# Kernel tuning notes

Measured on AMD Instinct MI355X. Metric: run time of the kernel, lower is better.

## Reference

```python
import jax, jax.numpy as jnp
import numpy as np

K = 256       # num states
M = 2         # markov order
D = 256       # lemb_size
V = 50000     # ntypes (vocab)
T = 512
B = 256
Kp1 = K + 1
EPS = 1e-5
INIT = 0.1


def _layernorm(h, g, b):
    mu = h.mean(-1, keepdims=True)
    var = ((h - mu) ** 2).mean(-1, keepdims=True)
    return (h - mu) / jnp.sqrt(var + EPS) * g + b


def setup_inputs() -> dict:
    key = jax.random.key(0)
    ks = jax.random.split(key, 12)
    u = lambda k, shp: jax.random.uniform(k, shp, jnp.float32, -INIT, INIT)
    return {
        "x": jax.random.randint(ks[0], (T, B), 0, V, dtype=jnp.int32),
        "z": jax.random.randint(ks[1], (T, B), 0, K, dtype=jnp.int32),
        "lembs": u(ks[2], (K, D)),
        "tlembs": u(ks[3], (Kp1, D)),
        "dec_W": u(ks[4], (V, D)),
        "dec_b": jnp.zeros((V,), jnp.float32),
        "em_W": u(ks[5], (D, D)),
        "em_bias": jnp.zeros((D,), jnp.float32),
        "em_g": jnp.ones((D,), jnp.float32),
        "em_beta": jnp.zeros((D,), jnp.float32),
        "td_W": u(ks[6], (K, M * D)),
        "td_b": jnp.zeros((K,), jnp.float32),
        "tm_W": u(ks[7], (M * D, M * D)),
        "tm_bias": jnp.zeros((M * D,), jnp.float32),
        "tn_g": jnp.ones((M * D,), jnp.float32),
        "tn_beta": jnp.zeros((M * D,), jnp.float32),
    }


def reference(x, z, lembs, tlembs, dec_W, dec_b, em_W, em_bias, em_g, em_beta,
              td_W, td_b, tm_W, tm_bias, tn_g, tn_beta):
    # --- emission distribution: K x V log-normalized ---
    h = _layernorm(lembs + jax.nn.relu(lembs @ em_W.T + em_bias), em_g, em_beta)
    emdist = jax.nn.log_softmax(h @ dec_W.T + dec_b, axis=1)  # (K, V)

    # --- transition distribution: (Kp1^M, K) log-normalized ---
    # cartesian product of label embeddings, row-major: row r <-> (i_0,...,i_{M-1})
    idx = jnp.indices((Kp1,) * M).reshape(M, -1)                 # (M, Kp1^M)
    cat = tlembs[idx].transpose(1, 0, 2).reshape(-1, M * D)      # (Kp1^M, M*D)
    th = _layernorm(cat + jax.nn.relu(cat @ tm_W.T + tm_bias), tn_g, tn_beta)
    transdist = jax.nn.log_softmax(th @ td_W.T + td_b, axis=1)   # (Kp1^M, K)

    # --- log_joint ---
    xlps = emdist.T[x]                                           # (T, B, K)
    emlps = jnp.take_along_axis(xlps, z[..., None].astype(jnp.int32), axis=2)[..., 0].sum(0)  # (B,)

    zpad = jnp.concatenate([jnp.full((M, B), K, dtype=z.dtype), z], axis=0)  # (T+M, B)
    win = jnp.stack([zpad[m:m + T] for m in range(M + 1)], 0)    # (M+1, T, B)
    lin = win[0]
    for m in range(1, M):
        lin = lin * Kp1 + win[m]                                 # row index into (Kp1^M, K)
    trans_lps = transdist[lin, win[M]]                           # (T, B)
    return emlps + trans_lps.sum(0)                              # (B,)
```

## Files before the change

### kernel.cpp

```cpp
#include <hip/hip_runtime.h>

#define Kst 256
#define Dd 256
#define Vv 50000
#define VPAD 50176
#define Tt 512
#define Bb 256
#define KP1 257
#define MD 512
#define NROWS (KP1*KP1)
#define EPSf 1e-5f

#define VB2 196
#define NP1 (VB2*4)
#define NTR ((NROWS+31)/32)
#define EMB 800

typedef __attribute__((ext_vector_type(8))) short short8;
typedef __attribute__((ext_vector_type(4))) float f32x4;
typedef __attribute__((ext_vector_type(4))) unsigned u32x4;
typedef __attribute__((ext_vector_type(2))) unsigned u32x2;

__device__ __forceinline__ unsigned short f2bf(float f) {
    unsigned u = __builtin_bit_cast(unsigned, f);
    unsigned r = (u + 0x7fffu + ((u >> 16) & 1u)) >> 16;
    return (unsigned short)r;
}
__device__ __forceinline__ float bf2f(unsigned short u) {
    return __builtin_bit_cast(float, ((unsigned)u) << 16);
}
__device__ __forceinline__ unsigned bfpack(float lo, float hi) {
    return __builtin_amdgcn_perm(__builtin_bit_cast(unsigned, hi),
                                 __builtin_bit_cast(unsigned, lo), 0x07060302u);
}
__device__ __forceinline__ unsigned f2bf2(float lo, float hi) {
    return (unsigned)f2bf(lo) | ((unsigned)f2bf(hi) << 16);
}

union HPU {
    struct { short ta[32][264]; float lsep[4][32][2]; float musig[32][2]; } g;
    struct { short pl[64][266]; } p;
};

__global__ __launch_bounds__(256) void k_hP(
    const float* __restrict__ lembs, const float* __restrict__ em_W,
    const float* __restrict__ em_bias, const float* __restrict__ em_g,
    const float* __restrict__ em_beta, unsigned short* __restrict__ h_bf,
    const float* __restrict__ tlembs, const float* __restrict__ tm_W,
    float* __restrict__ P0, float* __restrict__ P1,
    const float* __restrict__ td_W, const float* __restrict__ tn_g,
    const float* __restrict__ tn_beta, const float* __restrict__ td_b,
    unsigned short* __restrict__ tdwg_bf, float* __restrict__ Gt,
    float* __restrict__ Bt, const float* __restrict__ dec_W,
    unsigned short* __restrict__ dwP)
{
    __shared__ HPU su;
    int bid = blockIdx.x;
    int tid = threadIdx.x, lane = tid & 63, wv = tid >> 6;
    int l15 = lane & 15, q = lane >> 4;

    if (bid >= 108) {
        int pb = bid - 108;
        int vb2 = pb >> 2, c = pb & 3;
        short (*pl)[266] = su.p.pl;
        int base_row = vb2*256 + c*64;
        #pragma unroll 4
        for (int i = 0; i < 16; ++i) {
            int row = wv*16 + i;
            int grow = base_row + row; if (grow > Vv-1) grow = Vv-1;
            float4 f = ((const float4*)(dec_W + (size_t)grow*Dd))[lane];
            u32x2 w; w.x = bfpack(f.x, f.y); w.y = bfpack(f.z, f.w);
            *(u32x2*)&pl[row][lane*4] = w;
        }
        __syncthreads();
        #pragma unroll
        for (int i = 0; i < 8; ++i) {
            short8 val = *(const short8*)&pl[(lane & 15)*4 + wv][i*32 + (lane >> 4)*8];
            *(short8*)(dwP + ((size_t)vb2*8192 + (size_t)i*1024
                              + (c*4 + wv)*64 + lane)*8) = val;
        }
        return;
    }

    if (bid >= 44) {
        int c = (bid - 44)*4 + wv;
        const float4* w4 = (const float4*)(td_W + (size_t)c*MD);
        const float4* g4 = (const float4*)tn_g;
        const float4* b4 = (const float4*)tn_beta;
        float sg = 0.f, sb = 0.f;
        short8 o;
        #pragma unroll
        for (int u = 0; u < 2; ++u) {
            int j4 = lane*2 + u;
            float4 w = w4[j4], g = g4[j4], bt = b4[j4];
            sg += w.x*g.x + w.y*g.y + w.z*g.z + w.w*g.w;
            sb += w.x*bt.x + w.y*bt.y + w.z*bt.z + w.w*bt.w;
            o[u*4+0] = (short)f2bf(w.x*g.x);
            o[u*4+1] = (short)f2bf(w.y*g.y);
            o[u*4+2] = (short)f2bf(w.z*g.z);
            o[u*4+3] = (short)f2bf(w.w*g.w);
        }
        {
            int wvv = c >> 6, l15v = (c >> 2) & 15, ctv = c & 3;
            int ksv = lane >> 2, qv = lane & 3;
            *(short8*)(tdwg_bf +
                ((((size_t)wvv*16 + ksv)*4 + ctv)*64 + (qv*16 + l15v))*8) = o;
        }
        #pragma unroll
        for (int dd = 32; dd > 0; dd >>= 1) {
            sg += __shfl_xor(sg, dd);
            sb += __shfl_xor(sb, dd);
        }
        if (lane == 0) { Gt[c] = sg; Bt[c] = sb + td_b[c]; }
        return;
    }

    short (*ta)[264] = su.g.ta;
    float (*lsep)[32][2] = su.g.lsep;
    float (*musig)[2] = su.g.musig;

    int job, r0, cb, koff, BK;
    const float* Arow; const float* Brow;
    if (bid < 8) {
        job = 0; r0 = bid*32; cb = 0; koff = 0; BK = Dd;
        Arow = lembs; Brow = em_W;
    } else {
        int b2 = bid - 8;
        int half = b2 / 18;
        int b3 = b2 % 18;
        job = 1 + half;
        r0 = (b3 >> 1) * 32;
        cb = (b3 & 1) * 256;
        koff = half * 256; BK = MD;
        Arow = tlembs; Brow = tm_W;
    }

    {
        int row = tid >> 3, seg = (tid & 7) * 32;
        int r = r0 + row;
        if (r > 256) r = 256;
        const float4* s4 = (const float4*)(Arow + (size_t)r*Dd + seg);
        #pragma unroll
        for (int u = 0; u < 4; ++u) {
            float4 f0 = s4[u*2], f1 = s4[u*2+1];
            u32x4 pk;
            pk.x = bfpack(f0.x, f0.y);
            pk.y = bfpack(f0.z, f0.w);
            pk.z = bfpack(f1.x, f1.y);
            pk.w = bfpack(f1.z, f1.w);
            *(short8*)&ta[row][seg + u*8] = __builtin_bit_cast(short8, pk);
        }
    }
    __syncthreads();

    const float* bptr[4];
    #pragma unroll
    for (int ct = 0; ct < 4; ++ct) {
        int j = cb + wv*64 + ct*16 + l15;
        bptr[ct] = Brow + (size_t)j*BK + koff + q*8;
    }
    f32x4 acc[2][4];
    #pragma unroll
    for (int rt = 0; rt < 2; ++rt)
        #pragma unroll
        for (int ct = 0; ct < 4; ++ct)
            acc[rt][ct] = (f32x4){0.f,0.f,0.f,0.f};
    for (int ks = 0; ks < 8; ++ks) {
        short8 a0 = *(const short8*)&ta[ 0 + l15][ks*32 + q*8];
        short8 a1 = *(const short8*)&ta[16 + l15][ks*32 + q*8];
        short8 b[4];
        #pragma unroll
        for (int ct = 0; ct < 4; ++ct) {
            float4 f0 = *(const float4*)(bptr[ct] + ks*32);
            float4 f1 = *(const float4*)(bptr[ct] + ks*32 + 4);
            u32x4 pk;
            pk.x = bfpack(f0.x, f0.y);
            pk.y = bfpack(f0.z, f0.w);
            pk.z = bfpack(f1.x, f1.y);
            pk.w = bfpack(f1.z, f1.w);
            b[ct] = __builtin_bit_cast(short8, pk);
        }
        #pragma unroll
        for (int ct = 0; ct < 4; ++ct) {
            acc[0][ct] = __builtin_amdgcn_mfma_f32_16x16x32_bf16(a0, b[ct], acc[0][ct], 0,0,0);
            acc[1][ct] = __builtin_amdgcn_mfma_f32_16x16x32_bf16(a1, b[ct], acc[1][ct], 0,0,0);
        }
    }

    if (job != 0) {
        float* Pd = (job == 1) ? P0 : P1;
        #pragma unroll
        for (int rt = 0; rt < 2; ++rt) {
            #pragma unroll
            for (int reg = 0; reg < 4; ++reg) {
                int r = r0 + rt*16 + q*4 + reg;
                if (r < KP1) {
                    float* dst = Pd + (size_t)r*MD + cb + wv*64;
                    #pragma unroll
                    for (int ct = 0; ct < 4; ++ct)
                        dst[ct*16 + l15] = acc[rt][ct][reg];
                }
            }
        }
        return;
    }

    float bias_c[4];
    #pragma unroll
    for (int ct = 0; ct < 4; ++ct)
        bias_c[ct] = em_bias[wv*64 + ct*16 + l15];
    #pragma unroll
    for (int rt = 0; rt < 2; ++rt) {
        #pragma unroll
        for (int reg = 0; reg < 4; ++reg) {
            int r = r0 + rt*16 + q*4 + reg;
            #pragma unroll
            for (int ct = 0; ct < 4; ++ct) {
                float lv = lembs[(size_t)r*Dd + wv*64 + ct*16 + l15];
                acc[rt][ct][reg] = lv + fmaxf(acc[rt][ct][reg] + bias_c[ct], 0.f);
            }
        }
    }
    #pragma unroll
    for (int rt = 0; rt < 2; ++rt) {
        #pragma unroll
        for (int reg = 0; reg < 4; ++reg) {
            float s  = ((acc[rt][0][reg] + acc[rt][1][reg]) + (acc[rt][2][reg] + acc[rt][3][reg]));
            float ss = ((acc[rt][0][reg]*acc[rt][0][reg] + acc[rt][1][reg]*acc[rt][1][reg])
                      + (acc[rt][2][reg]*acc[rt][2][reg] + acc[rt][3][reg]*acc[rt][3][reg]));
            s  += __shfl_xor(s, 1);  ss += __shfl_xor(ss, 1);
            s  += __shfl_xor(s, 2);  ss += __shfl_xor(ss, 2);
            s  += __shfl_xor(s, 4);  ss += __shfl_xor(ss, 4);
            s  += __shfl_xor(s, 8);  ss += __shfl_xor(ss, 8);
            if (l15 == 0) {
                int rw = rt*16 + q*4 + reg;
                lsep[wv][rw][0] = s;
                lsep[wv][rw][1] = ss;
            }
        }
    }
    __syncthreads();
    if (tid < 32) {
        float s  = (lsep[0][tid][0] + lsep[1][tid][0]) + (lsep[2][tid][0] + lsep[3][tid][0]);
        float ss = (lsep[0][tid][1] + lsep[1][tid][1]) + (lsep[2][tid][1] + lsep[3][tid][1]);
        float mu = s * (1.f/Dd);
        musig[tid][0] = mu;
        musig[tid][1] = rsqrtf(ss*(1.f/Dd) - mu*mu + EPSf);
    }
    __syncthreads();
    float gl[4], bl[4];
    #pragma unroll
    for (int ct = 0; ct < 4; ++ct) {
        gl[ct] = em_g[wv*64 + ct*16 + l15];
        bl[ct] = em_beta[wv*64 + ct*16 + l15];
    }
    #pragma unroll
    for (int rt = 0; rt < 2; ++rt) {
        #pragma unroll
        for (int reg = 0; reg < 4; ++reg) {
            int rw = rt*16 + q*4 + reg;
            int r = r0 + rw;
            float mu = musig[rw][0], rs = musig[rw][1];
            unsigned short* dst = h_bf + (size_t)r*Dd + wv*64;
            #pragma unroll
            for (int ct = 0; ct < 4; ++ct)
                dst[ct*16 + l15] = f2bf((acc[rt][ct][reg] - mu)*rs*gl[ct] + bl[ct]);
        }
    }
}

union SMemU {
    struct { short hs[64][264]; } em;
    struct { short th[32][520]; float musig[32][2]; float lsep[4][32][2]; } tr;
};

__global__ __launch_bounds__(256, 4) void k_emtrans(
    const unsigned short* __restrict__ dwP, const float* __restrict__ dec_b,
    const unsigned short* __restrict__ h_bf, float* __restrict__ part1,
    unsigned short* __restrict__ E2,
    const float* __restrict__ tlembs, const float* __restrict__ P0,
    const float* __restrict__ P1, const float* __restrict__ tm_bias,
    const short* __restrict__ tdwg_bf, const float* __restrict__ Gt,
    const float* __restrict__ Bt, float* __restrict__ lse_t,
    unsigned short* __restrict__ Td)
{
    __shared__ SMemU sm;
    int bid = blockIdx.x;
    int tid = threadIdx.x, lane = tid & 63, wv = tid >> 6;
    int l15 = lane & 15, q = lane >> 4;

    if (bid < EMB) {
        int xcd = bid & 7, slot = bid >> 3;
        int g2 = slot >> 2, kg = slot & 3;
        int vb = g2*8 + xcd;
        if (vb >= VB2) return;
        short (*hs)[264] = sm.em.hs;

        {
            int row = tid >> 2, c0 = (tid & 3) * 64;
            const short8* src = (const short8*)(h_bf + (size_t)(kg*64 + row)*Dd + c0);
            #pragma unroll
            for (int u = 0; u < 8; ++u)
                *(short8*)&hs[row][c0 + u*8] = src[u];
        }
        __syncthreads();

        f32x4 acc[4][4];
        #pragma unroll
        for (int mt = 0; mt < 4; ++mt)
            #pragma unroll
            for (int ct = 0; ct < 4; ++ct)
                acc[mt][ct] = (f32x4){0.f,0.f,0.f,0.f};

        const short8* bb8 = (const short8*)dwP + ((size_t)vb*8*16 + wv*4)*64 + lane;
        short8 Bf[3][4];
        #define LDB_EM(slot_, kk) { \
            Bf[slot_][0] = bb8[((kk)*16 + 0)*64]; \
            Bf[slot_][1] = bb8[((kk)*16 + 1)*64]; \
            Bf[slot_][2] = bb8[((kk)*16 + 2)*64]; \
            Bf[slot_][3] = bb8[((kk)*16 + 3)*64]; }
        LDB_EM(0, 0)
        LDB_EM(1, 1)
        #pragma unroll
        for (int ks = 0; ks < 8; ++ks) {
            if (ks < 6) LDB_EM((ks+2)%3, ks+2)
            short8 a[4];
            #pragma unroll
            for (int mt = 0; mt < 4; ++mt)
                a[mt] = *(const short8*)&hs[mt*16 + l15][ks*32 + q*8];
            #pragma unroll
            for (int mt = 0; mt < 4; ++mt)
                #pragma unroll
                for (int ct = 0; ct < 4; ++ct)
                    acc[mt][ct] = __builtin_amdgcn_mfma_f32_16x16x32_bf16(a[mt], Bf[ks%3][ct], acc[mt][ct], 0,0,0);
        }
        #undef LDB_EM

        int vcol[4]; bool vok[4];
        #pragma unroll
        for (int ct = 0; ct < 4; ++ct) {
            int v = vb*256 + wv*64 + l15*4 + ct;
            vok[ct] = (v < Vv);
            vcol[ct] = v < Vv ? v : Vv-1;
        }
        #pragma unroll
        for (int ct = 0; ct < 4; ++ct) {
            if (vok[ct]) {
                float db = dec_b[vcol[ct]];
                #pragma unroll
                for (int mt = 0; mt < 4; ++mt)
                    #pragma unroll
                    for (int reg = 0; reg < 4; ++reg)
                        acc[mt][ct][reg] += db;
            } else {
                #pragma unroll
                for (int mt = 0; mt < 4; ++mt)
                    #pragma unroll
                    for (int reg = 0; reg < 4; ++reg)
                        acc[mt][ct][reg] = -1e30f;
            }
        }
        #pragma unroll
        for (int mt = 0; mt < 4; ++mt) {
            #pragma unroll
            for (int reg = 0; reg < 4; ++reg) {
                int k = kg*64 + mt*16 + q*4 + reg;
                u32x2 p;
                p.x = f2bf2(acc[mt][0][reg], acc[mt][1][reg]);
                p.y = f2bf2(acc[mt][2][reg], acc[mt][3][reg]);
                *(u32x2*)(E2 + (size_t)k*VPAD + vb*256 + wv*64 + l15*4) = p;
            }
        }
        #pragma unroll
        for (int mt = 0; mt < 4; ++mt) {
            #pragma unroll
            for (int reg = 0; reg < 4; ++reg) {
                float s = (__expf(acc[mt][0][reg]) + __expf(acc[mt][1][reg]))
                        + (__expf(acc[mt][2][reg]) + __expf(acc[mt][3][reg]));
                s += __shfl_xor(s, 1);
                s += __shfl_xor(s, 2);
                s += __shfl_xor(s, 4);
                s += __shfl_xor(s, 8);
                if (l15 == 0) {
                    int k = kg*64 + mt*16 + q*4 + reg;
                    part1[(size_t)(vb*4 + wv)*256 + k] = s;
                }
            }
        }
        return;
    }

    int tr_id = bid - EMB;
    if (tr_id >= NTR) return;
    short (*th)[520]   = sm.tr.th;
    float (*musig)[2]  = sm.tr.musig;
    float (*lsep)[32][2] = sm.tr.lsep;
    int r0 = tr_id * 32;

    {
        const float4* bias0 = (const float4*)tm_bias;
        const float4* bias1 = (const float4*)(tm_bias + 256);
        float4 c0 = bias0[lane], c1 = bias1[lane];
        int i0a[8], i1a[8];
        #pragma unroll
        for (int i = 0; i < 8; ++i) {
            int r = r0 + wv*8 + i; if (r >= NROWS) r = NROWS - 1;
            i0a[i] = r / KP1; i1a[i] = r - i0a[i]*KP1;
        }
        #define ROWBODY(i, A0, B0, T0, A1, B1, T1) { \
            int row = wv*8 + (i); \
            float v0 = (T0).x + fmaxf((A0).x+(B0).x+c0.x, 0.f); \
            float v1 = (T0).y + fmaxf((A0).y+(B0).y+c0.y, 0.f); \
            float v2 = (T0).z + fmaxf((A0).z+(B0).z+c0.z, 0.f); \
            float v3 = (T0).w + fmaxf((A0).w+(B0).w+c0.w, 0.f); \
            float v4 = (T1).x + fmaxf((A1).x+(B1).x+c1.x, 0.f); \
            float v5 = (T1).y + fmaxf((A1).y+(B1).y+c1.y, 0.f); \
            float v6 = (T1).z + fmaxf((A1).z+(B1).z+c1.z, 0.f); \
            float v7 = (T1).w + fmaxf((A1).w+(B1).w+c1.w, 0.f); \
            u32x2 p0; p0.x = bfpack(v0, v1); p0.y = bfpack(v2, v3); \
            u32x2 p1; p1.x = bfpack(v4, v5); p1.y = bfpack(v6, v7); \
            *(u32x2*)&th[row][lane*4]       = p0; \
            *(u32x2*)&th[row][256 + lane*4] = p1; \
            float s  = ((v0+v1)+(v2+v3)) + ((v4+v5)+(v6+v7)); \
            float ss = ((v0*v0+v1*v1)+(v2*v2+v3*v3)) + ((v4*v4+v5*v5)+(v6*v6+v7*v7)); \
            _Pragma("unroll") \
            for (int d = 1; d < 64; d <<= 1) { \
                s  += __shfl_xor(s, d); \
                ss += __shfl_xor(ss, d); \
            } \
            if (lane == 0) { \
                float mu = s * (1.f/MD); \
                musig[row][0] = mu; \
                musig[row][1] = rsqrtf(ss*(1.f/MD) - mu*mu + EPSf); \
            } }

        if (i0a[0] == i0a[7]) {
            float4 A0 = ((const float4*)(P0 + (size_t)i0a[0]*MD))[lane];
            float4 A1 = ((const float4*)(P0 + (size_t)i0a[0]*MD + 256))[lane];
            float4 T0 = ((const float4*)(tlembs + (size_t)i0a[0]*Dd))[lane];
            #pragma unroll
            for (int i = 0; i < 8; ++i) {
                float4 b0 = ((const float4*)(P1 + (size_t)i1a[i]*MD))[lane];
                float4 b1 = ((const float4*)(P1 + (size_t)i1a[i]*MD + 256))[lane];
                float4 t1 = ((const float4*)(tlembs + (size_t)i1a[i]*Dd))[lane];
                ROWBODY(i, A0, b0, T0, A1, b1, t1)
            }
        } else {
            #pragma unroll
            for (int i = 0; i < 8; ++i) {
                float4 A0 = ((const float4*)(P0 + (size_t)i0a[i]*MD))[lane];
                float4 A1 = ((const float4*)(P0 + (size_t)i0a[i]*MD + 256))[lane];
                float4 T0 = ((const float4*)(tlembs + (size_t)i0a[i]*Dd))[lane];
                float4 b0 = ((const float4*)(P1 + (size_t)i1a[i]*MD))[lane];
                float4 b1 = ((const float4*)(P1 + (size_t)i1a[i]*MD + 256))[lane];
                float4 t1 = ((const float4*)(tlembs + (size_t)i1a[i]*Dd))[lane];
                ROWBODY(i, A0, b0, T0, A1, b1, t1)
            }
        }
        #undef ROWBODY
    }
    __syncthreads();

    f32x4 acc[2][4];
    #pragma unroll
    for (int rt = 0; rt < 2; ++rt)
        #pragma unroll
        for (int ct = 0; ct < 4; ++ct)
            acc[rt][ct] = (f32x4){0.f, 0.f, 0.f, 0.f};
    const short* bb = tdwg_bf + (size_t)wv*32768 + (size_t)lane*8;
    short8 Bf[3][4];
    #define LDB_TR(slot_, kk) { const short* nxt = bb + (size_t)(kk)*2048; \
        Bf[slot_][0] = *(const short8*)(nxt); \
        Bf[slot_][1] = *(const short8*)(nxt + 512); \
        Bf[slot_][2] = *(const short8*)(nxt + 1024); \
        Bf[slot_][3] = *(const short8*)(nxt + 1536); }
    LDB_TR(0, 0)
    LDB_TR(1, 1)
    #pragma unroll
    for (int ks = 0; ks < 16; ++ks) {
        if (ks < 14) LDB_TR((ks+2)%3, ks+2)
        int ko = ks*32 + q*8;
        short8 a0 = *(const short8*)&th[ 0 + l15][ko];
        short8 a1 = *(const short8*)&th[16 + l15][ko];
        acc[0][0] = __builtin_amdgcn_mfma_f32_16x16x32_bf16(a0, Bf[ks%3][0], acc[0][0], 0,0,0);
        acc[1][0] = __builtin_amdgcn_mfma_f32_16x16x32_bf16(a1, Bf[ks%3][0], acc[1][0], 0,0,0);
        acc[0][1] = __builtin_amdgcn_mfma_f32_16x16x32_bf16(a0, Bf[ks%3][1], acc[0][1], 0,0,0);
        acc[1][1] = __builtin_amdgcn_mfma_f32_16x16x32_bf16(a1, Bf[ks%3][1], acc[1][1], 0,0,0);
        acc[0][2] = __builtin_amdgcn_mfma_f32_16x16x32_bf16(a0, Bf[ks%3][2], acc[0][2], 0,0,0);
        acc[1][2] = __builtin_amdgcn_mfma_f32_16x16x32_bf16(a1, Bf[ks%3][2], acc[1][2], 0,0,0);
        acc[0][3] = __builtin_amdgcn_mfma_f32_16x16x32_bf16(a0, Bf[ks%3][3], acc[0][3], 0,0,0);
        acc[1][3] = __builtin_amdgcn_mfma_f32_16x16x32_bf16(a1, Bf[ks%3][3], acc[1][3], 0,0,0);
    }
    #undef LDB_TR

    float4 Gc = *(const float4*)(Gt + wv*64 + l15*4);
    float4 Bc = *(const float4*)(Bt + wv*64 + l15*4);
    #pragma unroll
    for (int rt = 0; rt < 2; ++rt) {
        #pragma unroll
        for (int reg = 0; reg < 4; ++reg) {
            int rw = rt*16 + q*4 + reg;
            float mu = musig[rw][0], rs = musig[rw][1];
            float e0 = rs*(acc[rt][0][reg] - mu*Gc.x) + Bc.x;
            float e1 = rs*(acc[rt][1][reg] - mu*Gc.y) + Bc.y;
            float e2 = rs*(acc[rt][2][reg] - mu*Gc.z) + Bc.z;
            float e3 = rs*(acc[rt][3][reg] - mu*Gc.w) + Bc.w;
            long r = (long)r0 + rw;
            if (r < NROWS) {
                u32x2 p;
                p.x = f2bf2(e0, e1);
                p.y = f2bf2(e2, e3);
                *(u32x2*)(Td + (size_t)r*Kst + wv*64 + l15*4) = p;
            }
            float m = fmaxf(fmaxf(e0, e1), fmaxf(e2, e3));
            m = fmaxf(m, __shfl_xor(m, 1));
            m = fmaxf(m, __shfl_xor(m, 2));
            m = fmaxf(m, __shfl_xor(m, 4));
            m = fmaxf(m, __shfl_xor(m, 8));
            float s = __expf(e0 - m) + __expf(e1 - m) + __expf(e2 - m) + __expf(e3 - m);
            s += __shfl_xor(s, 1);
            s += __shfl_xor(s, 2);
            s += __shfl_xor(s, 4);
            s += __shfl_xor(s, 8);
            if (l15 == 0) {
                lsep[wv][rw][0] = m;
                lsep[wv][rw][1] = s;
            }
        }
    }
    __syncthreads();
    if (tid < 32) {
        int r = r0 + tid;
        if (r < NROWS) {
            float m0 = lsep[0][tid][0], m1 = lsep[1][tid][0];
            float m2 = lsep[2][tid][0], m3 = lsep[3][tid][0];
            float mg = fmaxf(fmaxf(m0, m1), fmaxf(m2, m3));
            float s = lsep[0][tid][1]*__expf(m0-mg) + lsep[1][tid][1]*__expf(m1-mg)
                    + lsep[2][tid][1]*__expf(m2-mg) + lsep[3][tid][1]*__expf(m3-mg);
            lse_t[r] = mg + logf(s);
        }
    }
}

__global__ __launch_bounds__(256) void k_gather6(
    const int* __restrict__ x, const int* __restrict__ z,
    const unsigned short* __restrict__ E2, const float* __restrict__ part1,
    const unsigned short* __restrict__ Td, const float* __restrict__ lse_t,
    float* __restrict__ out)
{
    __shared__ float lemp[4][256];
    __shared__ float lem[256];
    int tid = threadIdx.x, lane = tid & 63, w = tid >> 6;

    {
        const f32x4* p4 = (const f32x4*)part1;
        f32x4 s4 = (f32x4){0.f,0.f,0.f,0.f};
        int j0 = w*196;
        #pragma unroll 4
        for (int j = 0; j < 196; ++j) {
            f32x4 v = p4[(size_t)(j0 + j)*64 + lane];
            s4.x += v.x; s4.y += v.y; s4.z += v.z; s4.w += v.w;
        }
        *(f32x4*)&lemp[w][lane*4] = s4;
    }
    __syncthreads();
    lem[tid] = logf((lemp[0][tid] + lemp[1][tid]) + (lemp[2][tid] + lemp[3][tid]));
    __syncthreads();

    int b = blockIdx.x*4 + w;
    float accv = 0.f;
    #pragma unroll
    for (int u = 0; u < 8; ++u) {
        int t = u*64 + lane;
        int zc = z[t*Bb + b];
        int xv = x[t*Bb + b];
        int i0 = (t >= 2) ? z[(t-2)*Bb + b] : Kst;
        int i1 = (t >= 1) ? z[(t-1)*Bb + b] : Kst;
        int lin = i0*KP1 + i1;
        accv += bf2f(E2[(size_t)zc*VPAD + xv]) - lem[zc]
              + bf2f(Td[(size_t)lin*Kst + zc]) - lse_t[lin];
    }
    #pragma unroll
    for (int d = 1; d < 64; d <<= 1)
        accv += __shfl_xor(accv, d);
    if (lane == 0) out[b] = accv;
}

extern "C" void kernel_launch(void* const* d_in, const int* in_sizes, int n_in,
                              void* d_out, int out_size, void* d_ws, size_t ws_size,
                              hipStream_t stream)
{
    const int*   x       = (const int*)  d_in[0];
    const int*   z       = (const int*)  d_in[1];
    const float* lembs   = (const float*)d_in[2];
    const float* tlembs  = (const float*)d_in[3];
    const float* dec_W   = (const float*)d_in[4];
    const float* dec_b   = (const float*)d_in[5];
    const float* em_W    = (const float*)d_in[6];
    const float* em_bias = (const float*)d_in[7];
    const float* em_g    = (const float*)d_in[8];
    const float* em_beta = (const float*)d_in[9];
    const float* td_W    = (const float*)d_in[10];
    const float* td_b    = (const float*)d_in[11];
    const float* tm_W    = (const float*)d_in[12];
    const float* tm_bias = (const float*)d_in[13];
    const float* tn_g    = (const float*)d_in[14];
    const float* tn_beta = (const float*)d_in[15];
    float* out = (float*)d_out;

    float* ws     = (float*)d_ws;
    float* P0     = ws;
    float* P1     = P0 + 131584;
    float* part1  = P1 + 131584;
    float* lse_t  = part1 + 200704;
    float* Gt     = lse_t + 66052;
    float* Bt     = Gt + 256;
    unsigned short* tdwg_bf = (unsigned short*)(Bt + 256);
    unsigned short* h_bf   = tdwg_bf + 131072;
    unsigned short* E2     = h_bf + 65536;
    unsigned short* Td     = E2 + (size_t)Kst*VPAD;
    unsigned short* dwP    = Td + (size_t)NROWS*Kst;

    k_hP<<<108 + 784, 256, 0, stream>>>(lembs, em_W, em_bias, em_g, em_beta, h_bf,
                                        tlembs, tm_W, P0, P1,
                                        td_W, tn_g, tn_beta, td_b, tdwg_bf, Gt, Bt,
                                        dec_W, dwP);
    k_emtrans<<<EMB + NTR, 256, 0, stream>>>(
        dwP, dec_b, h_bf, part1, E2,
        tlembs, P0, P1, tm_bias, (const short*)tdwg_bf, Gt, Bt, lse_t, Td);
    k_gather6<<<64, 256, 0, stream>>>(x, z, E2, part1, Td, lse_t, out);
}
```

Before: 220.1 us.

## Split final gather into partial-LSE, time-tiled gather, and finish kernels; prefetch rows

```diff
diff --git a/kernel.cpp b/kernel.cpp
--- a/kernel.cpp
+++ b/kernel.cpp
@@ -438,23 +438,40 @@
             float4 A0 = ((const float4*)(P0 + (size_t)i0a[0]*MD))[lane];
             float4 A1 = ((const float4*)(P0 + (size_t)i0a[0]*MD + 256))[lane];
             float4 T0 = ((const float4*)(tlembs + (size_t)i0a[0]*Dd))[lane];
+            float4 b0 = ((const float4*)(P1 + (size_t)i1a[0]*MD))[lane];
+            float4 b1 = ((const float4*)(P1 + (size_t)i1a[0]*MD + 256))[lane];
+            float4 t1 = ((const float4*)(tlembs + (size_t)i1a[0]*Dd))[lane];
             #pragma unroll
             for (int i = 0; i < 8; ++i) {
-                float4 b0 = ((const float4*)(P1 + (size_t)i1a[i]*MD))[lane];
-                float4 b1 = ((const float4*)(P1 + (size_t)i1a[i]*MD + 256))[lane];
-                float4 t1 = ((const float4*)(tlembs + (size_t)i1a[i]*Dd))[lane];
+                float4 nb0, nb1, nt1;
+                if (i < 7) {
+                    nb0 = ((const float4*)(P1 + (size_t)i1a[i+1]*MD))[lane];
+                    nb1 = ((const float4*)(P1 + (size_t)i1a[i+1]*MD + 256))[lane];
+                    nt1 = ((const float4*)(tlembs + (size_t)i1a[i+1]*Dd))[lane];
+                }
                 ROWBODY(i, A0, b0, T0, A1, b1, t1)
+                b0 = nb0; b1 = nb1; t1 = nt1;
             }
         } else {
+            float4 A0 = ((const float4*)(P0 + (size_t)i0a[0]*MD))[lane];
+            float4 A1 = ((const float4*)(P0 + (size_t)i0a[0]*MD + 256))[lane];
+            float4 T0 = ((const float4*)(tlembs + (size_t)i0a[0]*Dd))[lane];
+            float4 b0 = ((const float4*)(P1 + (size_t)i1a[0]*MD))[lane];
+            float4 b1 = ((const float4*)(P1 + (size_t)i1a[0]*MD + 256))[lane];
+            float4 t1 = ((const float4*)(tlembs + (size_t)i1a[0]*Dd))[lane];
             #pragma unroll
             for (int i = 0; i < 8; ++i) {
-                float4 A0 = ((const float4*)(P0 + (size_t)i0a[i]*MD))[lane];
-                float4 A1 = ((const float4*)(P0 + (size_t)i0a[i]*MD + 256))[lane];
-                float4 T0 = ((const float4*)(tlembs + (size_t)i0a[i]*Dd))[lane];
-                float4 b0 = ((const float4*)(P1 + (size_t)i1a[i]*MD))[lane];
-                float4 b1 = ((const float4*)(P1 + (size_t)i1a[i]*MD + 256))[lane];
-                float4 t1 = ((const float4*)(tlembs + (size_t)i1a[i]*Dd))[lane];
+                float4 nA0, nA1, nT0, nb0, nb1, nt1;
+                if (i < 7) {
+                    nA0 = ((const float4*)(P0 + (size_t)i0a[i+1]*MD))[lane];
+                    nA1 = ((const float4*)(P0 + (size_t)i0a[i+1]*MD + 256))[lane];
+                    nT0 = ((const float4*)(tlembs + (size_t)i0a[i+1]*Dd))[lane];
+                    nb0 = ((const float4*)(P1 + (size_t)i1a[i+1]*MD))[lane];
+                    nb1 = ((const float4*)(P1 + (size_t)i1a[i+1]*MD + 256))[lane];
+                    nt1 = ((const float4*)(tlembs + (size_t)i1a[i+1]*Dd))[lane];
+                }
                 ROWBODY(i, A0, b0, T0, A1, b1, t1)
+                A0 = nA0; A1 = nA1; T0 = nT0; b0 = nb0; b1 = nb1; t1 = nt1;
             }
         }
         #undef ROWBODY
@@ -542,48 +559,66 @@
     }
 }
 
-__global__ __launch_bounds__(256) void k_gather6(
-    const int* __restrict__ x, const int* __restrict__ z,
-    const unsigned short* __restrict__ E2, const float* __restrict__ part1,
-    const unsigned short* __restrict__ Td, const float* __restrict__ lse_t,
-    float* __restrict__ out)
+__global__ __launch_bounds__(256) void k_lse8(
+    const float* __restrict__ part1, float* __restrict__ lpart)
 {
     __shared__ float lemp[4][256];
+    int tid = threadIdx.x, lane = tid & 63, w = tid >> 6;
+    const f32x4* p4 = (const f32x4*)part1;
+    f32x4 s4 = (f32x4){0.f,0.f,0.f,0.f};
+    int j0 = blockIdx.x * 98;
+    for (int j = j0 + w; j < j0 + 98; j += 4) {
+        f32x4 v = p4[(size_t)j*64 + lane];
+        s4.x += v.x; s4.y += v.y; s4.z += v.z; s4.w += v.w;
+    }
+    *(f32x4*)&lemp[w][lane*4] = s4;
+    __syncthreads();
+    lpart[blockIdx.x*256 + tid] = (lemp[0][tid] + lemp[1][tid]) + (lemp[2][tid] + lemp[3][tid]);
+}
+
+__global__ __launch_bounds__(256) void k_gather7(
+    const int* __restrict__ x, const int* __restrict__ z,
+    const unsigned short* __restrict__ E2, const float* __restrict__ lpart,
+    const unsigned short* __restrict__ Td, const float* __restrict__ lse_t,
+    float* __restrict__ gpart)
+{
     __shared__ float lem[256];
-    int tid = threadIdx.x, lane = tid & 63, w = tid >> 6;
-
+    int tid = threadIdx.x;
     {
-        const f32x4* p4 = (const f32x4*)part1;
-        f32x4 s4 = (f32x4){0.f,0.f,0.f,0.f};
-        int j0 = w*196;
-        #pragma unroll 4
-        for (int j = 0; j < 196; ++j) {
-            f32x4 v = p4[(size_t)(j0 + j)*64 + lane];
-            s4.x += v.x; s4.y += v.y; s4.z += v.z; s4.w += v.w;
-        }
-        *(f32x4*)&lemp[w][lane*4] = s4;
+        float s = 0.f;
+        #pragma unroll
+        for (int r = 0; r < 8; ++r) s += lpart[r*256 + tid];
+        lem[tid] = logf(s);
     }
     __syncthreads();
-    lem[tid] = logf((lemp[0][tid] + lemp[1][tid]) + (lemp[2][tid] + lemp[3][tid]));
-    __syncthreads();
-
-    int b = blockIdx.x*4 + w;
+
+    int b = tid;
+    int t0 = blockIdx.x * 8;
+    int zm1 = (t0 >= 1) ? z[(t0-1)*Bb + b] : Kst;
+    int zm2 = (t0 >= 2) ? z[(t0-2)*Bb + b] : Kst;
     float accv = 0.f;
     #pragma unroll
     for (int u = 0; u < 8; ++u) {
-        int t = u*64 + lane;
+        int t = t0 + u;
         int zc = z[t*Bb + b];
         int xv = x[t*Bb + b];
-        int i0 = (t >= 2) ? z[(t-2)*Bb + b] : Kst;
-        int i1 = (t >= 1) ? z[(t-1)*Bb + b] : Kst;
-        int lin = i0*KP1 + i1;
+        int lin = zm2*KP1 + zm1;
         accv += bf2f(E2[(size_t)zc*VPAD + xv]) - lem[zc]
               + bf2f(Td[(size_t)lin*Kst + zc]) - lse_t[lin];
-    }
-    #pragma unroll
-    for (int d = 1; d < 64; d <<= 1)
-        accv += __shfl_xor(accv, d);
-    if (lane == 0) out[b] = accv;
+        zm2 = zm1; zm1 = zc;
+    }
+    gpart[blockIdx.x*Bb + b] = accv;
+}
+
+__global__ __launch_bounds__(256) void k_fin(
+    const float* __restrict__ gpart, float* __restrict__ out)
+{
+    int b = threadIdx.x;
+    float s = 0.f;
+    #pragma unroll 8
+    for (int r = 0; r < 64; ++r)
+        s += gpart[r*Bb + b];
+    out[b] = s;
 }
 
 extern "C" void kernel_launch(void* const* d_in, const int* in_sizes, int n_in,
@@ -612,7 +647,9 @@
     float* P0     = ws;
     float* P1     = P0 + 131584;
     float* part1  = P1 + 131584;
-    float* lse_t  = part1 + 200704;
+    float* lpart  = part1 + 200704;
+    float* gpart  = lpart + 2048;
+    float* lse_t  = gpart + 16384;
     float* Gt     = lse_t + 66052;
     float* Bt     = Gt + 256;
     unsigned short* tdwg_bf = (unsigned short*)(Bt + 256);
@@ -628,5 +665,7 @@
     k_emtrans<<<EMB + NTR, 256, 0, stream>>>(
         dwP, dec_b, h_bf, part1, E2,
         tlembs, P0, P1, tm_bias, (const short*)tdwg_bf, Gt, Bt, lse_t, Td);
-    k_gather6<<<64, 256, 0, stream>>>(x, z, E2, part1, Td, lse_t, out);
-}
+    k_lse8<<<8, 256, 0, stream>>>(part1, lpart);
+    k_gather7<<<64, 256, 0, stream>>>(x, z, E2, lpart, Td, lse_t, gpart);
+    k_fin<<<1, 256, 0, stream>>>(gpart, out);
+}
```

Measured after the change: 203.6 us. 7.5% less time.
